# Kernel optimization log

Hardware: AMD Instinct MI355X
Metric: run time of the kernel (lower is better)

The kernel has to match this reference:

```python
import jax, jax.numpy as jnp
import numpy as np

B, N, D, E = 64, 1000, 128, 20000
NEG_SLOPE = 0.2   # GraphLayer leaky_relu negative_slope
BN_EPS = 1e-5


def setup_inputs() -> dict:
    key = jax.random.key(0)
    ks = jax.random.split(key, 16)
    data = jax.random.normal(ks[0], (B, N, D), jnp.float32)
    # edges with no self-loops (GraphLayer removes self-loops before re-adding them)
    dst = jax.random.randint(ks[1], (E,), 0, N)
    off = jax.random.randint(ks[2], (E,), 1, N)
    src = (dst + off) % N
    edge_index = jnp.stack([src, dst]).astype(jnp.int32)  # [2, E], row0=src(j), row1=dst(i)

    def p(k, shape, scale=0.05):
        return jax.random.normal(k, shape, jnp.float32) * scale

    return dict(
        data=data, edge_index=edge_index,
        emb=p(ks[3], (N, D), 0.1),
        lin_w=p(ks[4], (D, D)),
        att_i=p(ks[5], (D,)), att_j=p(ks[6], (D,)),
        att_em_i=p(ks[7], (D,)), att_em_j=p(ks[8], (D,)),
        gnn_bias=jnp.zeros((D,), jnp.float32),
        bn_gamma=jnp.ones((D,), jnp.float32),
        bn_beta=jnp.zeros((D,), jnp.float32),
        q_w=p(ks[9], (D, D)), q_b=jnp.zeros((D,), jnp.float32),
        k_w=p(ks[10], (D, D)), k_b=jnp.zeros((D,), jnp.float32),
        v_w=p(ks[11], (D, D)), v_b=jnp.zeros((D,), jnp.float32),
        temperature=jnp.asarray(np.sqrt(D), jnp.float32),
        f_w1=p(ks[12], (D, 2 * D)), f_b1=jnp.zeros((D,), jnp.float32),
        f_w2=p(ks[13], (D, D)), f_b2=jnp.zeros((D,), jnp.float32),
        out_w=p(ks[14], (1, D)), out_b=jnp.zeros((1,), jnp.float32),
    )


def _forward(data, emb, lin_w, att_i, att_j, att_em_i, att_em_j, gnn_bias,
             bn_gamma, bn_beta, q_w, q_b, k_w, k_b, v_w, v_b, temperature,
             f_w1, f_b1, f_w2, f_b2, out_w, out_b, edge_index):
    Bn = B * N
    # ---- temporal self-attention (seq_len == dim -> window of 1, per code constraint)
    xt = data.reshape(B, N, -1, D)                           # [B, N, W, D]
    q = xt @ q_w.T + q_b
    k = xt @ k_w.T + k_b
    v = xt @ v_w.T + v_b
    scores = jnp.einsum('bnwc,bnuc->bnwu', q, k) / (temperature + 1e-6)
    attn = jax.nn.softmax(scores, axis=-1)
    t_out = jnp.einsum('bnwu,bnuc->bnwc', attn, v).reshape(B, N, -1)

    # ---- spatial graph attention (GDN GraphLayer, heads=1, concat=False)
    x = data.reshape(Bn, -1) @ lin_w.T                       # [Bn, D]
    offs = jnp.arange(B, dtype=edge_index.dtype) * N         # get_batch_edge_index
    src = (edge_index[0][None, :] + offs[:, None]).reshape(-1)
    dst = (edge_index[1][None, :] + offs[:, None]).reshape(-1)
    loop = jnp.arange(Bn, dtype=edge_index.dtype)            # add_self_loops
    src = jnp.concatenate([src, loop])
    dst = jnp.concatenate([dst, loop])
    emb_full = jnp.tile(emb, (B, 1))                         # embedding tiled per graph
    # alpha_e = <[x_i|emb_i],[att_i|att_em_i]> + <[x_j|emb_j],[att_j|att_em_j]>
    node_i_score = x @ att_i + emb_full @ att_em_i           # [Bn]
    node_j_score = x @ att_j + emb_full @ att_em_j
    alpha = node_i_score[dst] + node_j_score[src]            # [E_total]
    alpha = jnp.where(alpha >= 0, alpha, NEG_SLOPE * alpha)  # leaky_relu(0.2)
    amax = jax.ops.segment_max(alpha, dst, num_segments=Bn)  # segment softmax over targets
    ex = jnp.exp(alpha - amax[dst])
    denom = jax.ops.segment_sum(ex, dst, num_segments=Bn)
    w = ex / denom[dst]
    agg = jax.ops.segment_sum(x[src] * w[:, None], dst, num_segments=Bn) + gnn_bias
    # BatchNorm1d (training-mode batch statistics, biased var) + ReLU
    mu = agg.mean(axis=0)
    var = agg.var(axis=0)
    s_out = jax.nn.relu(bn_gamma * (agg - mu) * jax.lax.rsqrt(var + BN_EPS) + bn_beta)
    s_out = s_out.reshape(B, N, -1)

    # ---- fusion MLP + OutLayer (layer_num=1 -> single Linear(D, 1))
    combined = jnp.concatenate([s_out, t_out], axis=-1)      # [B, N, 2D]
    fused = jax.nn.relu(combined @ f_w1.T + f_b1) @ f_w2.T + f_b2
    out = fused @ out_w.T + out_b                            # [B, N, 1]
    return out.reshape(Bn)


def reference(data, edge_index, emb, lin_w, att_i, att_j, att_em_i, att_em_j,
              gnn_bias, bn_gamma, bn_beta, q_w, q_b, k_w, k_b, v_w, v_b,
              temperature, f_w1, f_b1, f_w2, f_b2, out_w, out_b):
    return _forward(data, emb, lin_w, att_i, att_j, att_em_i, att_em_j, gnn_bias,
                    bn_gamma, bn_beta, q_w, q_b, k_w, k_b, v_w, v_b, temperature,
                    f_w1, f_b1, f_w2, f_b2, out_w, out_b, edge_index)
```

## Files before the change

kernel.cpp:

```cpp
#include <hip/hip_runtime.h>
#include <math.h>

constexpr int B_ = 64;
constexpr int N_ = 1000;
constexpr int D_ = 128;
constexpr int E_ = 20000;
constexpr int BN_TOT = B_ * N_;
constexpr float BN_EPS = 1e-5f;
constexpr float NEG_SLOPE = 0.2f;

typedef __attribute__((ext_vector_type(8))) __bf16 bf16x8;
typedef __attribute__((ext_vector_type(4))) float f32x4;
typedef __attribute__((ext_vector_type(2))) float f32x2;
typedef __attribute__((ext_vector_type(2))) unsigned int u32x2;

__device__ __forceinline__ float leaky(float a) { return a >= 0.f ? a : NEG_SLOPE * a; }

__device__ __forceinline__ bf16x8 cvt8(const float* v) {
    bf16x8 h;
#pragma unroll
    for (int j = 0; j < 8; ++j) h[j] = (__bf16)v[j];
    return h;
}

__device__ __forceinline__ unsigned int pack2(float a, float b) {
    __bf16 b0 = (__bf16)a, b1 = (__bf16)b;
    unsigned int u0 = *(const unsigned short*)&b0;
    unsigned int u1 = *(const unsigned short*)&b1;
    return u0 | (u1 << 16);
}

__device__ __forceinline__ unsigned int packpair(float v, int l) {
    float vp = __shfl_xor(v, 1);
    return pack2(v, vp);
}

__global__ __launch_bounds__(256) void k_prep(const float* __restrict__ lin_w,
                                              const float* __restrict__ v_w,
                                              const float* __restrict__ f_w1,
                                              const float* __restrict__ emb,
                                              const float* __restrict__ att_em_i,
                                              const float* __restrict__ att_em_j,
                                              const float* __restrict__ f_w2,
                                              const float* __restrict__ f_b2,
                                              const float* __restrict__ out_w,
                                              const float* __restrict__ out_b,
                                              __bf16* __restrict__ wcat_h, __bf16* __restrict__ wcat_l,
                                              __bf16* __restrict__ f1_h, __bf16* __restrict__ f1_l,
                                              float* __restrict__ eemi, float* __restrict__ eemj,
                                              float* __restrict__ g, float* __restrict__ c0,
                                              int* __restrict__ zbase) {
    const int blk = blockIdx.x;
    const int tid = threadIdx.x;
    if (blk < 256) {
        int i = blk * 256 + tid;
        if (i < 32768) {
            float v = (i < 16384) ? lin_w[i] : v_w[i - 16384];
            __bf16 h = (__bf16)v;
            wcat_h[i] = h;
            wcat_l[i] = (__bf16)(v - (float)h);
        } else {
            int j = i - 32768;
            float v = f_w1[j];
            __bf16 h = (__bf16)v;
            f1_h[j] = h;
            f1_l[j] = (__bf16)(v - (float)h);
        }
    } else if (blk == 256) {
        for (int k = tid; k < 2304; k += 256) zbase[k] = 0;
    } else if (blk == 257) {
        if (tid < 128) {
            float s = 0.f;
            for (int k = 0; k < D_; ++k) s += out_w[k] * f_w2[k * D_ + tid];
            g[tid] = s;
            if (tid == 0) {
                float c = out_b[0];
                for (int k = 0; k < D_; ++k) c += out_w[k] * f_b2[k];
                *c0 = c;
            }
        }
    } else {
        const int wid = tid >> 6;
        const int lane = tid & 63;
        const int n = (blk - 258) * 4 + wid;
        const float* er = emb + (size_t)n * D_;
        float e0 = er[lane], e1 = er[lane + 64];
        float si = e0 * att_em_i[lane] + e1 * att_em_i[lane + 64];
        float sj = e0 * att_em_j[lane] + e1 * att_em_j[lane + 64];
        for (int off = 32; off > 0; off >>= 1) {
            si += __shfl_down(si, off);
            sj += __shfl_down(sj, off);
        }
        if (lane == 0) { eemi[n] = si; eemj[n] = sj; }
    }
}

__global__ void k_count(const int* __restrict__ ei, int* __restrict__ offs) {
    int e = blockIdx.x * blockDim.x + threadIdx.x;
    if (e < E_) atomicAdd(&offs[ei[E_ + e] + 1], 1);
}

__global__ __launch_bounds__(1024) void k_scan(int* __restrict__ offs) {
    __shared__ int s[N_ + 1];
    int tid = threadIdx.x;
    if (tid <= N_) s[tid] = offs[tid];
    __syncthreads();
    for (int off = 1; off <= N_; off <<= 1) {
        int v = 0;
        if (tid <= N_) { v = s[tid]; if (tid >= off) v += s[tid - off]; }
        __syncthreads();
        if (tid <= N_) s[tid] = v;
        __syncthreads();
    }
    if (tid <= N_) offs[tid] = s[tid];
}

__global__ void k_scatter(const int* __restrict__ ei, const int* __restrict__ offs,
                          int* __restrict__ cursor, int* __restrict__ csr_src) {
    int e = blockIdx.x * blockDim.x + threadIdx.x;
    if (e < E_) {
        int dn = ei[E_ + e];
        int pos = offs[dn] + atomicAdd(&cursor[dn], 1);
        csr_src[pos] = ei[e];
    }
}

__global__ __launch_bounds__(512) void k_mfma_dual(const float* __restrict__ data,
                                                   const __bf16* __restrict__ wcat_h,
                                                   const __bf16* __restrict__ wcat_l,
                                                   const float* __restrict__ v_b,
                                                   const float* __restrict__ att_i,
                                                   const float* __restrict__ att_j,
                                                   const float* __restrict__ eemi,
                                                   const float* __restrict__ eemj,
                                                   float* __restrict__ ni,
                                                   float* __restrict__ nj,
                                                   unsigned int* __restrict__ xb,
                                                   unsigned int* __restrict__ tb) {
    const int tid = threadIdx.x;
    const int w = tid >> 6;
    const int l = tid & 63;
    bf16x8 Bh[2][4], Bl[2][4];
#pragma unroll
    for (int nt = 0; nt < 2; ++nt) {
        const int n = w * 32 + nt * 16 + (l & 15);
#pragma unroll
        for (int kk = 0; kk < 4; ++kk) {
            const int k = kk * 32 + (l >> 4) * 8;
            Bh[nt][kk] = *(const bf16x8*)&wcat_h[n * D_ + k];
            Bl[nt][kk] = *(const bf16x8*)&wcat_l[n * D_ + k];
        }
    }
    float vb[2] = {0.f, 0.f};
    float ai[2] = {0.f, 0.f}, aj[2] = {0.f, 0.f};
    if (w >= 4) {
#pragma unroll
        for (int nt = 0; nt < 2; ++nt) vb[nt] = v_b[w * 32 + nt * 16 + (l & 15) - 128];
    } else {
#pragma unroll
        for (int nt = 0; nt < 2; ++nt) {
            const int col = w * 32 + nt * 16 + (l & 15);
            ai[nt] = att_i[col];
            aj[nt] = att_j[col];
        }
    }
    __shared__ __align__(16) __bf16 dh[2][32 * D_];
    __shared__ float sred_i[4][32];
    __shared__ float sred_j[4][32];
    const int srow = tid >> 4;
    const int skq = (tid & 15) * 8;
    const int soff = srow * D_ + (skq ^ ((srow & 7) * 8));
    const int nchunks = BN_TOT / 32;
    float4 q0, q1;
    {
        const float* src = data + (size_t)(blockIdx.x * 32 + srow) * D_ + skq;
        q0 = *(const float4*)src;
        q1 = *(const float4*)(src + 4);
        float v[8] = {q0.x, q0.y, q0.z, q0.w, q1.x, q1.y, q1.z, q1.w};
        *(bf16x8*)&dh[0][soff] = cvt8(v);
    }
    int cur = 0;
    for (int ch = blockIdx.x; ch < nchunks; ch += gridDim.x) {
        const int nxt = ch + gridDim.x;
        if (nxt < nchunks) {
            const float* src = data + (size_t)(nxt * 32 + srow) * D_ + skq;
            q0 = *(const float4*)src;
            q1 = *(const float4*)(src + 4);
        }
        __syncthreads();
        f32x4 acc[2][2];
#pragma unroll
        for (int mt = 0; mt < 2; ++mt)
#pragma unroll
            for (int nt = 0; nt < 2; ++nt) acc[mt][nt] = (f32x4){0.f, 0.f, 0.f, 0.f};
#pragma unroll
        for (int mt = 0; mt < 2; ++mt) {
#pragma unroll
            for (int kk = 0; kk < 4; ++kk) {
                const int aidx = (mt * 16 + (l & 15)) * D_ + ((kk * 32 + (l >> 4) * 8) ^ ((l & 7) * 8));
                bf16x8 ah = *(const bf16x8*)&dh[cur][aidx];
#pragma unroll
                for (int nt = 0; nt < 2; ++nt) {
                    acc[mt][nt] = __builtin_amdgcn_mfma_f32_16x16x32_bf16(ah, Bh[nt][kk], acc[mt][nt], 0, 0, 0);
                    acc[mt][nt] = __builtin_amdgcn_mfma_f32_16x16x32_bf16(ah, Bl[nt][kk], acc[mt][nt], 0, 0, 0);
                }
            }
        }
        const int row0 = ch * 32;
        if (w < 4) {
            float pi[8], pj[8];
#pragma unroll
            for (int k2 = 0; k2 < 8; ++k2) { pi[k2] = 0.f; pj[k2] = 0.f; }
#pragma unroll
            for (int mt = 0; mt < 2; ++mt) {
#pragma unroll
                for (int nt = 0; nt < 2; ++nt) {
                    const int col = w * 32 + nt * 16 + (l & 15);
#pragma unroll
                    for (int r = 0; r < 4; ++r) {
                        float v = acc[mt][nt][r];
                        pi[mt * 4 + r] += v * ai[nt];
                        pj[mt * 4 + r] += v * aj[nt];
                        unsigned int u = packpair(v, l);
                        if (!(l & 1)) {
                            const int row = row0 + mt * 16 + (l >> 4) * 4 + r;
                            xb[(size_t)row * 64 + (col >> 1)] = u;
                        }
                    }
                }
            }
#pragma unroll
            for (int off = 1; off < 16; off <<= 1) {
#pragma unroll
                for (int k2 = 0; k2 < 8; ++k2) {
                    pi[k2] += __shfl_xor(pi[k2], off);
                    pj[k2] += __shfl_xor(pj[k2], off);
                }
            }
            if ((l & 15) == 0) {
#pragma unroll
                for (int mt = 0; mt < 2; ++mt)
#pragma unroll
                    for (int r = 0; r < 4; ++r) {
                        sred_i[w][mt * 16 + (l >> 4) * 4 + r] = pi[mt * 4 + r];
                        sred_j[w][mt * 16 + (l >> 4) * 4 + r] = pj[mt * 4 + r];
                    }
            }
        } else {
#pragma unroll
            for (int mt = 0; mt < 2; ++mt) {
#pragma unroll
                for (int nt = 0; nt < 2; ++nt) {
                    const int c2 = w * 32 + nt * 16 + (l & 15) - 128;
#pragma unroll
                    for (int r = 0; r < 4; ++r) {
                        float v = acc[mt][nt][r] + vb[nt];
                        unsigned int u = packpair(v, l);
                        if (!(l & 1)) {
                            const int row = row0 + mt * 16 + (l >> 4) * 4 + r;
                            tb[(size_t)row * 64 + (c2 >> 1)] = u;
                        }
                    }
                }
            }
        }
        __syncthreads();
        if (tid < 32) {
            const int row = row0 + tid;
            float si = sred_i[0][tid] + sred_i[1][tid] + sred_i[2][tid] + sred_i[3][tid];
            float sj = sred_j[0][tid] + sred_j[1][tid] + sred_j[2][tid] + sred_j[3][tid];
            const int n = row % N_;
            ni[row] = si + eemi[n];
            nj[row] = sj + eemj[n];
        }
        if (nxt < nchunks) {
            float v[8] = {q0.x, q0.y, q0.z, q0.w, q1.x, q1.y, q1.z, q1.w};
            *(bf16x8*)&dh[cur ^ 1][soff] = cvt8(v);
        }
        cur ^= 1;
    }
}

__global__ __launch_bounds__(256) void k_sagg(const unsigned int* __restrict__ xb,
                                              const int* __restrict__ offs,
                                              const int* __restrict__ csr_src,
                                              const float* __restrict__ ni,
                                              const float* __restrict__ nj,
                                              const float* __restrict__ gnn_bias,
                                              unsigned int* __restrict__ ab,
                                              float* __restrict__ partials) {
    constexpr int CAP = 128;
    __shared__ int s_lds[4][CAP];
    __shared__ float w_lds[4][CAP];
    __shared__ f32x4 bns[4][32];
    __shared__ f32x4 bnq[4][32];
    const int swz = (blockIdx.x & 7) * 2000 + (blockIdx.x >> 3);
    const int w = threadIdx.x >> 6;
    const int l = threadIdx.x & 63;
    const int bid = swz * 4 + w;
    const int b = bid / N_;
    const int i = bid - b * N_;
    const int base = b * N_;
    const int e0 = offs[i];
    const int deg = offs[i + 1] - e0;
    const int stg = deg < CAP ? deg : CAP;
    const float nii = ni[bid];
    const float aself = leaky(nii + nj[bid]);
    float aa0 = -1e30f, aa1 = -1e30f;
    if (l < stg) {
        int s = csr_src[e0 + l];
        s_lds[w][l] = s;
        aa0 = leaky(nii + nj[base + s]);
    }
    if (l + 64 < stg) {
        int s = csr_src[e0 + l + 64];
        s_lds[w][l + 64] = s;
        aa1 = leaky(nii + nj[base + s]);
    }
    float amax = fmaxf(aself, fmaxf(aa0, aa1));
    for (int e = e0 + CAP + l; e < e0 + deg; e += 64)
        amax = fmaxf(amax, leaky(nii + nj[base + csr_src[e]]));
    for (int off = 32; off > 0; off >>= 1) amax = fmaxf(amax, __shfl_xor(amax, off));
    const float se = __expf(aself - amax);
    float sum = 0.f;
    if (l < stg) { float ex = __expf(aa0 - amax); w_lds[w][l] = ex; sum += ex; }
    if (l + 64 < stg) { float ex = __expf(aa1 - amax); w_lds[w][l + 64] = ex; sum += ex; }
    for (int off = 32; off > 0; off >>= 1) sum += __shfl_xor(sum, off);
    float denom = se + sum;
    __syncthreads();
    const int hw = l >> 5;
    const int c = l & 31;
    const uint2* x2 = (const uint2*)xb;
    f32x2 a01 = (f32x2){0.f, 0.f}, a23 = (f32x2){0.f, 0.f};
    if (hw == 0) {
        uint2 u = x2[(size_t)bid * 32 + c];
        f32x2 v01, v23;
        v01.x = __uint_as_float(u.x << 16); v01.y = __uint_as_float(u.x & 0xffff0000u);
        v23.x = __uint_as_float(u.y << 16); v23.y = __uint_as_float(u.y & 0xffff0000u);
        a01 += se * v01;
        a23 += se * v23;
    }
    int k = 0;
    for (; k + 8 <= stg; k += 8) {
        uint2 u[4];
        float wg[4];
#pragma unroll
        for (int j = 0; j < 4; ++j) {
            int e = k + j * 2 + hw;
            int s = s_lds[w][e];
            wg[j] = w_lds[w][e];
            u[j] = x2[(size_t)(base + s) * 32 + c];
        }
#pragma unroll
        for (int j = 0; j < 4; ++j) {
            f32x2 v01, v23;
            v01.x = __uint_as_float(u[j].x << 16); v01.y = __uint_as_float(u[j].x & 0xffff0000u);
            v23.x = __uint_as_float(u[j].y << 16); v23.y = __uint_as_float(u[j].y & 0xffff0000u);
            a01 += wg[j] * v01;
            a23 += wg[j] * v23;
        }
    }
    for (; k + 2 <= stg; k += 2) {
        int e = k + hw;
        int s = s_lds[w][e];
        float wg = w_lds[w][e];
        uint2 u = x2[(size_t)(base + s) * 32 + c];
        f32x2 v01, v23;
        v01.x = __uint_as_float(u.x << 16); v01.y = __uint_as_float(u.x & 0xffff0000u);
        v23.x = __uint_as_float(u.y << 16); v23.y = __uint_as_float(u.y & 0xffff0000u);
        a01 += wg * v01;
        a23 += wg * v23;
    }
    if (k < stg && hw == 0) {
        int s = s_lds[w][k];
        float wg = w_lds[w][k];
        uint2 u = x2[(size_t)(base + s) * 32 + c];
        f32x2 v01, v23;
        v01.x = __uint_as_float(u.x << 16); v01.y = __uint_as_float(u.x & 0xffff0000u);
        v23.x = __uint_as_float(u.y << 16); v23.y = __uint_as_float(u.y & 0xffff0000u);
        a01 += wg * v01;
        a23 += wg * v23;
    }
    for (int e = e0 + CAP; e < e0 + deg; ++e) {
        int s = csr_src[e];
        float wg = __expf(leaky(nii + nj[base + s]) - amax);
        if (hw == 0) {
            uint2 u = x2[(size_t)(base + s) * 32 + c];
            f32x2 v01, v23;
            v01.x = __uint_as_float(u.x << 16); v01.y = __uint_as_float(u.x & 0xffff0000u);
            v23.x = __uint_as_float(u.y << 16); v23.y = __uint_as_float(u.y & 0xffff0000u);
            a01 += wg * v01;
            a23 += wg * v23;
        }
        denom += wg;
    }
    a01.x += __shfl_xor(a01.x, 32);
    a01.y += __shfl_xor(a01.y, 32);
    a23.x += __shfl_xor(a23.x, 32);
    a23.y += __shfl_xor(a23.y, 32);
    if (hw == 0) {
        const float dn = 1.f / denom;
        f32x4 gb = ((const f32x4*)gnn_bias)[c];
        f32x4 o;
        o.x = a01.x * dn + gb.x;
        o.y = a01.y * dn + gb.y;
        o.z = a23.x * dn + gb.z;
        o.w = a23.y * dn + gb.w;
        u32x2 u;
        u.x = pack2(o.x, o.y);
        u.y = pack2(o.z, o.w);
        __builtin_nontemporal_store(u, (u32x2*)ab + (size_t)bid * 32 + c);
        bns[w][c] = o;
        bnq[w][c] = o * o;
    }
    __syncthreads();
    if (threadIdx.x < 32) {
        const int cc = threadIdx.x;
        f32x4 s = bns[0][cc] + bns[1][cc] + bns[2][cc] + bns[3][cc];
        f32x4 q = bnq[0][cc] + bnq[1][cc] + bnq[2][cc] + bnq[3][cc];
        f32x4* p = (f32x4*)partials + (size_t)blockIdx.x * 64;
        p[cc] = s;
        p[32 + cc] = q;
    }
}

__global__ __launch_bounds__(256) void k_bn_redA(const float* __restrict__ partials,
                                                 float* __restrict__ partial2) {
    const int t = threadIdx.x;
    float s = 0.f;
    const int r0 = blockIdx.x * 125;
    for (int r = r0; r < r0 + 125; ++r)
        s += partials[(size_t)r * 256 + t];
    partial2[(size_t)blockIdx.x * 256 + t] = s;
}

__global__ __launch_bounds__(256) void k_bn_finB(const float* __restrict__ partial2,
                                                 const float* __restrict__ gamma,
                                                 const float* __restrict__ beta,
                                                 float* __restrict__ scale,
                                                 float* __restrict__ shift) {
    const int t = threadIdx.x;
    float s = 0.f;
    for (int r = 0; r < 128; ++r) s += partial2[(size_t)r * 256 + t];
    __shared__ float tot[256];
    tot[t] = s;
    __syncthreads();
    if (t < 128) {
        float mu = tot[t] * (1.f / BN_TOT);
        float var = tot[128 + t] * (1.f / BN_TOT) - mu * mu;
        float sc = gamma[t] * rsqrtf(var + BN_EPS);
        scale[t] = sc;
        shift[t] = beta[t] - mu * sc;
    }
}

__global__ __launch_bounds__(512) void k_mfma_fusion(const unsigned int* __restrict__ ab,
                                                     const unsigned int* __restrict__ tb,
                                                     const __bf16* __restrict__ f1_h,
                                                     const __bf16* __restrict__ f1_l,
                                                     const float* __restrict__ f_b1,
                                                     const float* __restrict__ scale,
                                                     const float* __restrict__ shift,
                                                     const float* __restrict__ g,
                                                     const float* __restrict__ c0p,
                                                     float* __restrict__ out) {
    const int tid = threadIdx.x;
    const int w = tid >> 6;
    const int l = tid & 63;
    const float c0v = *c0p;
    bf16x8 Fh[8], Fl[8];
    const int ncol = w * 16 + (l & 15);
#pragma unroll
    for (int kk = 0; kk < 8; ++kk) {
        const int k = kk * 32 + (l >> 4) * 8;
        Fh[kk] = *(const bf16x8*)&f1_h[ncol * 256 + k];
        Fl[kk] = *(const bf16x8*)&f1_l[ncol * 256 + k];
    }
    const float b1c = f_b1[ncol];
    const float gc = g[ncol];
    __shared__ __align__(16) __bf16 ch_[2][32 * 256];
    __shared__ float part[8][32];
    const int srow = tid >> 4;
    const int scb = (tid & 15) * 16;
    const bool isagg = scb < 128;
    float4 sc4[4], sh4[4];
    if (isagg) {
#pragma unroll
        for (int q = 0; q < 4; ++q) {
            sc4[q] = *(const float4*)&scale[scb + q * 4];
            sh4[q] = *(const float4*)&shift[scb + q * 4];
        }
    }
    const unsigned int* basep = isagg ? ab : tb;
    const int uoff = (scb & 127) >> 1;
    const int nchunks = BN_TOT / 32;
    uint4 qu[2];
    auto loadc = [&](int chk) {
        const unsigned int* srcp = basep + (size_t)(chk * 32 + srow) * 64 + uoff;
        qu[0] = *(const uint4*)srcp;
        qu[1] = *(const uint4*)(srcp + 4);
    };
    auto storec = [&](int buf) {
        if (isagg) {
            float v[16];
            unsigned int us[8] = {qu[0].x, qu[0].y, qu[0].z, qu[0].w,
                                  qu[1].x, qu[1].y, qu[1].z, qu[1].w};
#pragma unroll
            for (int j = 0; j < 8; ++j) {
                v[j * 2 + 0] = __uint_as_float(us[j] << 16);
                v[j * 2 + 1] = __uint_as_float(us[j] & 0xffff0000u);
            }
#pragma unroll
            for (int qq = 0; qq < 4; ++qq) {
                v[qq * 4 + 0] = fmaxf(v[qq * 4 + 0] * sc4[qq].x + sh4[qq].x, 0.f);
                v[qq * 4 + 1] = fmaxf(v[qq * 4 + 1] * sc4[qq].y + sh4[qq].y, 0.f);
                v[qq * 4 + 2] = fmaxf(v[qq * 4 + 2] * sc4[qq].z + sh4[qq].z, 0.f);
                v[qq * 4 + 3] = fmaxf(v[qq * 4 + 3] * sc4[qq].w + sh4[qq].w, 0.f);
            }
#pragma unroll
            for (int hh = 0; hh < 2; ++hh) {
                const int c = scb + hh * 8;
                const int idx = srow * 256 + (c ^ ((srow & 7) * 8));
                *(bf16x8*)&ch_[buf][idx] = cvt8(v + hh * 8);
            }
        } else {
#pragma unroll
            for (int hh = 0; hh < 2; ++hh) {
                const int c = scb + hh * 8;
                const int idx = srow * 256 + (c ^ ((srow & 7) * 8));
                *(bf16x8*)&ch_[buf][idx] = *(const bf16x8*)&qu[hh];
            }
        }
    };
    loadc(blockIdx.x);
    storec(0);
    int cur = 0;
    for (int chk = blockIdx.x; chk < nchunks; chk += gridDim.x) {
        const int nxt = chk + gridDim.x;
        if (nxt < nchunks) loadc(nxt);
        __syncthreads();
#pragma unroll
        for (int mt = 0; mt < 2; ++mt) {
            f32x4 acc = (f32x4){0.f, 0.f, 0.f, 0.f};
#pragma unroll
            for (int kk = 0; kk < 8; ++kk) {
                const int ai = (mt * 16 + (l & 15)) * 256 + ((kk * 32 + (l >> 4) * 8) ^ ((l & 7) * 8));
                bf16x8 ah = *(const bf16x8*)&ch_[cur][ai];
                acc = __builtin_amdgcn_mfma_f32_16x16x32_bf16(ah, Fh[kk], acc, 0, 0, 0);
                acc = __builtin_amdgcn_mfma_f32_16x16x32_bf16(ah, Fl[kk], acc, 0, 0, 0);
            }
            float p[4];
#pragma unroll
            for (int r = 0; r < 4; ++r) p[r] = fmaxf(acc[r] + b1c, 0.f) * gc;
#pragma unroll
            for (int r = 0; r < 4; ++r) {
                p[r] += __shfl_xor(p[r], 1);
                p[r] += __shfl_xor(p[r], 2);
                p[r] += __shfl_xor(p[r], 4);
                p[r] += __shfl_xor(p[r], 8);
            }
            if ((l & 15) == 0) {
#pragma unroll
                for (int r = 0; r < 4; ++r) part[w][mt * 16 + (l >> 4) * 4 + r] = p[r];
            }
        }
        __syncthreads();
        if (tid < 32) {
            float s = c0v;
#pragma unroll
            for (int ww = 0; ww < 8; ++ww) s += part[ww][tid];
            out[chk * 32 + tid] = s;
        }
        if (nxt < nchunks) storec(cur ^ 1);
        cur ^= 1;
    }
}

extern "C" void kernel_launch(void* const* d_in, const int* in_sizes, int n_in,
                              void* d_out, int out_size, void* d_ws, size_t ws_size,
                              hipStream_t stream) {
    const float* data     = (const float*)d_in[0];
    const int*   ei       = (const int*)d_in[1];
    const float* emb      = (const float*)d_in[2];
    const float* lin_w    = (const float*)d_in[3];
    const float* att_i    = (const float*)d_in[4];
    const float* att_j    = (const float*)d_in[5];
    const float* att_em_i = (const float*)d_in[6];
    const float* att_em_j = (const float*)d_in[7];
    const float* gnn_bias = (const float*)d_in[8];
    const float* bn_gamma = (const float*)d_in[9];
    const float* bn_beta  = (const float*)d_in[10];
    const float* v_w      = (const float*)d_in[15];
    const float* v_b      = (const float*)d_in[16];
    const float* f_w1     = (const float*)d_in[18];
    const float* f_b1     = (const float*)d_in[19];
    const float* f_w2     = (const float*)d_in[20];
    const float* f_b2     = (const float*)d_in[21];
    const float* out_w    = (const float*)d_in[22];
    const float* out_b    = (const float*)d_in[23];
    float* out = (float*)d_out;

    float* ws = (float*)d_ws;
    float* x      = ws;
    float* tmat   = x + (size_t)BN_TOT * D_;
    float* aggr   = tmat + (size_t)BN_TOT * D_;
    float* ni     = aggr + (size_t)BN_TOT * D_;
    float* nj     = ni + BN_TOT;
    float* eemi   = nj + BN_TOT;
    float* eemj   = eemi + N_;
    float* g      = eemj + N_;
    float* c0     = g + D_;
    float* scale  = c0 + 8;
    float* shift  = scale + D_;
    int* offs     = (int*)(shift + D_);
    int* cursor   = offs + 1024;
    float* bn_sum = (float*)(cursor + 1024);
    float* bn_sq  = bn_sum + D_;
    int* csr_src  = (int*)(bn_sq + D_);
    float* partials = (float*)(csr_src + E_);
    float* partial2 = partials + (size_t)16000 * 256;
    __bf16* wcat_h = (__bf16*)(partial2 + 128 * 256);
    __bf16* wcat_l = wcat_h + 256 * 128;
    __bf16* f1_h   = wcat_l + 256 * 128;
    __bf16* f1_l   = f1_h + 128 * 256;
    unsigned int* xb = (unsigned int*)(f1_l + 128 * 256);
    unsigned int* tb = (unsigned int*)tmat;
    unsigned int* ab = (unsigned int*)aggr;

    k_prep<<<508, 256, 0, stream>>>(lin_w, v_w, f_w1, emb, att_em_i, att_em_j,
                                    f_w2, f_b2, out_w, out_b,
                                    wcat_h, wcat_l, f1_h, f1_l,
                                    eemi, eemj, g, c0, offs);
    k_count<<<(E_ + 255) / 256, 256, 0, stream>>>(ei, offs);
    k_scan<<<1, 1024, 0, stream>>>(offs);
    k_scatter<<<(E_ + 255) / 256, 256, 0, stream>>>(ei, offs, cursor, csr_src);
    k_mfma_dual<<<500, 512, 0, stream>>>(data, wcat_h, wcat_l, v_b,
                                         att_i, att_j, eemi, eemj,
                                         ni, nj, xb, tb);
    k_sagg<<<BN_TOT / 4, 256, 0, stream>>>(xb, offs, csr_src, ni, nj, gnn_bias, ab, partials);
    k_bn_redA<<<128, 256, 0, stream>>>(partials, partial2);
    k_bn_finB<<<1, 256, 0, stream>>>(partial2, bn_gamma, bn_beta, scale, shift);
    k_mfma_fusion<<<500, 512, 0, stream>>>(ab, tb, f1_h, f1_l, f_b1, scale, shift, g, c0, out);
}
```

Measured before the change: 135.6 us.

## Build CSR in one kernel and widen gather loads in aggregation

Replaces the count, scan and scatter kernels, plus the zeroing step in the prep kernel, with a single one-block kernel that builds the CSR using LDS histogram and cursor arrays, removing launches and global atomics. The spatial aggregation kernel now has each lane load 16 bytes (8 bf16) of a neighbour row, so a wave processes four edges per step instead of two, with a two-stage shuffle reduction. It also drops a __syncthreads before the gather. The single-block CSR build runs serially on one CU.

```diff
diff --git a/kernel.cpp b/kernel.cpp
--- a/kernel.cpp
+++ b/kernel.cpp
@@ -12,7 +12,7 @@
 typedef __attribute__((ext_vector_type(8))) __bf16 bf16x8;
 typedef __attribute__((ext_vector_type(4))) float f32x4;
 typedef __attribute__((ext_vector_type(2))) float f32x2;
-typedef __attribute__((ext_vector_type(2))) unsigned int u32x2;
+typedef __attribute__((ext_vector_type(4))) unsigned int u32x4;
 
 __device__ __forceinline__ float leaky(float a) { return a >= 0.f ? a : NEG_SLOPE * a; }
 
@@ -33,6 +33,19 @@
 __device__ __forceinline__ unsigned int packpair(float v, int l) {
     float vp = __shfl_xor(v, 1);
     return pack2(v, vp);
+}
+
+__device__ __forceinline__ void acc8(u32x4 u, float wg,
+                                     f32x2& a0, f32x2& a1, f32x2& a2, f32x2& a3) {
+    f32x2 v;
+    v.x = __uint_as_float(u.x << 16); v.y = __uint_as_float(u.x & 0xffff0000u);
+    a0 += wg * v;
+    v.x = __uint_as_float(u.y << 16); v.y = __uint_as_float(u.y & 0xffff0000u);
+    a1 += wg * v;
+    v.x = __uint_as_float(u.z << 16); v.y = __uint_as_float(u.z & 0xffff0000u);
+    a2 += wg * v;
+    v.x = __uint_as_float(u.w << 16); v.y = __uint_as_float(u.w & 0xffff0000u);
+    a3 += wg * v;
 }
 
 __global__ __launch_bounds__(256) void k_prep(const float* __restrict__ lin_w,
@@ -48,8 +61,7 @@
                                               __bf16* __restrict__ wcat_h, __bf16* __restrict__ wcat_l,
                                               __bf16* __restrict__ f1_h, __bf16* __restrict__ f1_l,
                                               float* __restrict__ eemi, float* __restrict__ eemj,
-                                              float* __restrict__ g, float* __restrict__ c0,
-                                              int* __restrict__ zbase) {
+                                              float* __restrict__ g, float* __restrict__ c0) {
     const int blk = blockIdx.x;
     const int tid = threadIdx.x;
     if (blk < 256) {
@@ -67,8 +79,6 @@
             f1_l[j] = (__bf16)(v - (float)h);
         }
     } else if (blk == 256) {
-        for (int k = tid; k < 2304; k += 256) zbase[k] = 0;
-    } else if (blk == 257) {
         if (tid < 128) {
             float s = 0.f;
             for (int k = 0; k < D_; ++k) s += out_w[k] * f_w2[k * D_ + tid];
@@ -82,7 +92,7 @@
     } else {
         const int wid = tid >> 6;
         const int lane = tid & 63;
-        const int n = (blk - 258) * 4 + wid;
+        const int n = (blk - 257) * 4 + wid;
         const float* er = emb + (size_t)n * D_;
         float e0 = er[lane], e1 = er[lane + 64];
         float si = e0 * att_em_i[lane] + e1 * att_em_i[lane + 64];
@@ -95,32 +105,29 @@
     }
 }
 
-__global__ void k_count(const int* __restrict__ ei, int* __restrict__ offs) {
-    int e = blockIdx.x * blockDim.x + threadIdx.x;
-    if (e < E_) atomicAdd(&offs[ei[E_ + e] + 1], 1);
-}
-
-__global__ __launch_bounds__(1024) void k_scan(int* __restrict__ offs) {
-    __shared__ int s[N_ + 1];
-    int tid = threadIdx.x;
-    if (tid <= N_) s[tid] = offs[tid];
+__global__ __launch_bounds__(1024) void k_csr(const int* __restrict__ ei,
+                                              int* __restrict__ offs,
+                                              int* __restrict__ csr_src) {
+    __shared__ int hist[N_ + 1];
+    __shared__ int cur[N_];
+    const int tid = threadIdx.x;
+    for (int i = tid; i <= N_; i += 1024) hist[i] = 0;
+    __syncthreads();
+    for (int e = tid; e < E_; e += 1024) atomicAdd(&hist[ei[E_ + e] + 1], 1);
     __syncthreads();
     for (int off = 1; off <= N_; off <<= 1) {
         int v = 0;
-        if (tid <= N_) { v = s[tid]; if (tid >= off) v += s[tid - off]; }
+        if (tid <= N_) { v = hist[tid]; if (tid >= off) v += hist[tid - off]; }
         __syncthreads();
-        if (tid <= N_) s[tid] = v;
+        if (tid <= N_) hist[tid] = v;
         __syncthreads();
     }
-    if (tid <= N_) offs[tid] = s[tid];
-}
-
-__global__ void k_scatter(const int* __restrict__ ei, const int* __restrict__ offs,
-                          int* __restrict__ cursor, int* __restrict__ csr_src) {
-    int e = blockIdx.x * blockDim.x + threadIdx.x;
-    if (e < E_) {
+    if (tid <= N_) offs[tid] = hist[tid];
+    for (int i = tid; i < N_; i += 1024) cur[i] = 0;
+    __syncthreads();
+    for (int e = tid; e < E_; e += 1024) {
         int dn = ei[E_ + e];
-        int pos = offs[dn] + atomicAdd(&cursor[dn], 1);
+        int pos = hist[dn] + atomicAdd(&cur[dn], 1);
         csr_src[pos] = ei[e];
     }
 }
@@ -327,91 +334,70 @@
     if (l + 64 < stg) { float ex = __expf(aa1 - amax); w_lds[w][l + 64] = ex; sum += ex; }
     for (int off = 32; off > 0; off >>= 1) sum += __shfl_xor(sum, off);
     float denom = se + sum;
-    __syncthreads();
-    const int hw = l >> 5;
-    const int c = l & 31;
-    const uint2* x2 = (const uint2*)xb;
-    f32x2 a01 = (f32x2){0.f, 0.f}, a23 = (f32x2){0.f, 0.f};
-    if (hw == 0) {
-        uint2 u = x2[(size_t)bid * 32 + c];
-        f32x2 v01, v23;
-        v01.x = __uint_as_float(u.x << 16); v01.y = __uint_as_float(u.x & 0xffff0000u);
-        v23.x = __uint_as_float(u.y << 16); v23.y = __uint_as_float(u.y & 0xffff0000u);
-        a01 += se * v01;
-        a23 += se * v23;
+    const int qw = l >> 4;
+    const int c = l & 15;
+    const u32x4* x4 = (const u32x4*)xb;
+    f32x2 a0 = (f32x2){0.f, 0.f}, a1 = (f32x2){0.f, 0.f};
+    f32x2 a2 = (f32x2){0.f, 0.f}, a3 = (f32x2){0.f, 0.f};
+    if (qw == 0) {
+        u32x4 u = x4[(size_t)bid * 16 + c];
+        acc8(u, se, a0, a1, a2, a3);
     }
     int k = 0;
     for (; k + 8 <= stg; k += 8) {
-        uint2 u[4];
-        float wg[4];
-#pragma unroll
-        for (int j = 0; j < 4; ++j) {
-            int e = k + j * 2 + hw;
-            int s = s_lds[w][e];
-            wg[j] = w_lds[w][e];
-            u[j] = x2[(size_t)(base + s) * 32 + c];
-        }
-#pragma unroll
-        for (int j = 0; j < 4; ++j) {
-            f32x2 v01, v23;
-            v01.x = __uint_as_float(u[j].x << 16); v01.y = __uint_as_float(u[j].x & 0xffff0000u);
-            v23.x = __uint_as_float(u[j].y << 16); v23.y = __uint_as_float(u[j].y & 0xffff0000u);
-            a01 += wg[j] * v01;
-            a23 += wg[j] * v23;
-        }
-    }
-    for (; k + 2 <= stg; k += 2) {
-        int e = k + hw;
+        int e1_ = k + qw, e2_ = k + 4 + qw;
+        int s1 = s_lds[w][e1_], s2 = s_lds[w][e2_];
+        float wg1 = w_lds[w][e1_], wg2 = w_lds[w][e2_];
+        u32x4 u1 = x4[(size_t)(base + s1) * 16 + c];
+        u32x4 u2 = x4[(size_t)(base + s2) * 16 + c];
+        acc8(u1, wg1, a0, a1, a2, a3);
+        acc8(u2, wg2, a0, a1, a2, a3);
+    }
+    for (; k + 4 <= stg; k += 4) {
+        int e = k + qw;
         int s = s_lds[w][e];
         float wg = w_lds[w][e];
-        uint2 u = x2[(size_t)(base + s) * 32 + c];
-        f32x2 v01, v23;
-        v01.x = __uint_as_float(u.x << 16); v01.y = __uint_as_float(u.x & 0xffff0000u);
-        v23.x = __uint_as_float(u.y << 16); v23.y = __uint_as_float(u.y & 0xffff0000u);
-        a01 += wg * v01;
-        a23 += wg * v23;
-    }
-    if (k < stg && hw == 0) {
-        int s = s_lds[w][k];
-        float wg = w_lds[w][k];
-        uint2 u = x2[(size_t)(base + s) * 32 + c];
-        f32x2 v01, v23;
-        v01.x = __uint_as_float(u.x << 16); v01.y = __uint_as_float(u.x & 0xffff0000u);
-        v23.x = __uint_as_float(u.y << 16); v23.y = __uint_as_float(u.y & 0xffff0000u);
-        a01 += wg * v01;
-        a23 += wg * v23;
+        u32x4 u = x4[(size_t)(base + s) * 16 + c];
+        acc8(u, wg, a0, a1, a2, a3);
+    }
+    if (k + qw < stg) {
+        int e = k + qw;
+        int s = s_lds[w][e];
+        float wg = w_lds[w][e];
+        u32x4 u = x4[(size_t)(base + s) * 16 + c];
+        acc8(u, wg, a0, a1, a2, a3);
     }
     for (int e = e0 + CAP; e < e0 + deg; ++e) {
         int s = csr_src[e];
         float wg = __expf(leaky(nii + nj[base + s]) - amax);
-        if (hw == 0) {
-            uint2 u = x2[(size_t)(base + s) * 32 + c];
-            f32x2 v01, v23;
-            v01.x = __uint_as_float(u.x << 16); v01.y = __uint_as_float(u.x & 0xffff0000u);
-            v23.x = __uint_as_float(u.y << 16); v23.y = __uint_as_float(u.y & 0xffff0000u);
-            a01 += wg * v01;
-            a23 += wg * v23;
+        if (qw == 0) {
+            u32x4 u = x4[(size_t)(base + s) * 16 + c];
+            acc8(u, wg, a0, a1, a2, a3);
         }
         denom += wg;
     }
-    a01.x += __shfl_xor(a01.x, 32);
-    a01.y += __shfl_xor(a01.y, 32);
-    a23.x += __shfl_xor(a23.x, 32);
-    a23.y += __shfl_xor(a23.y, 32);
-    if (hw == 0) {
+#pragma unroll
+    for (int off = 16; off <= 32; off <<= 1) {
+        a0.x += __shfl_xor(a0.x, off); a0.y += __shfl_xor(a0.y, off);
+        a1.x += __shfl_xor(a1.x, off); a1.y += __shfl_xor(a1.y, off);
+        a2.x += __shfl_xor(a2.x, off); a2.y += __shfl_xor(a2.y, off);
+        a3.x += __shfl_xor(a3.x, off); a3.y += __shfl_xor(a3.y, off);
+    }
+    if (qw == 0) {
         const float dn = 1.f / denom;
-        f32x4 gb = ((const f32x4*)gnn_bias)[c];
-        f32x4 o;
-        o.x = a01.x * dn + gb.x;
-        o.y = a01.y * dn + gb.y;
-        o.z = a23.x * dn + gb.z;
-        o.w = a23.y * dn + gb.w;
-        u32x2 u;
-        u.x = pack2(o.x, o.y);
-        u.y = pack2(o.z, o.w);
-        __builtin_nontemporal_store(u, (u32x2*)ab + (size_t)bid * 32 + c);
-        bns[w][c] = o;
-        bnq[w][c] = o * o;
+        const f32x4* gb4 = (const f32x4*)gnn_bias;
+        f32x4 o0, o1;
+        f32x4 g0 = gb4[2 * c], g1 = gb4[2 * c + 1];
+        o0.x = a0.x * dn + g0.x; o0.y = a0.y * dn + g0.y;
+        o0.z = a1.x * dn + g0.z; o0.w = a1.y * dn + g0.w;
+        o1.x = a2.x * dn + g1.x; o1.y = a2.y * dn + g1.y;
+        o1.z = a3.x * dn + g1.z; o1.w = a3.y * dn + g1.w;
+        u32x4 up;
+        up.x = pack2(o0.x, o0.y); up.y = pack2(o0.z, o0.w);
+        up.z = pack2(o1.x, o1.y); up.w = pack2(o1.z, o1.w);
+        __builtin_nontemporal_store(up, (u32x4*)ab + (size_t)bid * 16 + c);
+        bns[w][2 * c] = o0;  bns[w][2 * c + 1] = o1;
+        bnq[w][2 * c] = o0 * o0;  bnq[w][2 * c + 1] = o1 * o1;
     }
     __syncthreads();
     if (threadIdx.x < 32) {
@@ -494,11 +480,11 @@
     const unsigned int* basep = isagg ? ab : tb;
     const int uoff = (scb & 127) >> 1;
     const int nchunks = BN_TOT / 32;
-    uint4 qu[2];
+    u32x4 qu[2];
     auto loadc = [&](int chk) {
         const unsigned int* srcp = basep + (size_t)(chk * 32 + srow) * 64 + uoff;
-        qu[0] = *(const uint4*)srcp;
-        qu[1] = *(const uint4*)(srcp + 4);
+        qu[0] = *(const u32x4*)srcp;
+        qu[1] = *(const u32x4*)(srcp + 4);
     };
     auto storec = [&](int buf) {
         if (isagg) {
@@ -627,13 +613,11 @@
     unsigned int* tb = (unsigned int*)tmat;
     unsigned int* ab = (unsigned int*)aggr;
 
-    k_prep<<<508, 256, 0, stream>>>(lin_w, v_w, f_w1, emb, att_em_i, att_em_j,
+    k_prep<<<507, 256, 0, stream>>>(lin_w, v_w, f_w1, emb, att_em_i, att_em_j,
                                     f_w2, f_b2, out_w, out_b,
                                     wcat_h, wcat_l, f1_h, f1_l,
-                                    eemi, eemj, g, c0, offs);
-    k_count<<<(E_ + 255) / 256, 256, 0, stream>>>(ei, offs);
-    k_scan<<<1, 1024, 0, stream>>>(offs);
-    k_scatter<<<(E_ + 255) / 256, 256, 0, stream>>>(ei, offs, cursor, csr_src);
+                                    eemi, eemj, g, c0);
+    k_csr<<<1, 1024, 0, stream>>>(ei, offs, csr_src);
     k_mfma_dual<<<500, 512, 0, stream>>>(data, wcat_h, wcat_l, v_b,
                                          att_i, att_j, eemi, eemj,
                                          ni, nj, xb, tb);
```

After: 147.0 us. 8.4% more time.
